# Kernel optimization log

Measured on AMD Instinct MI355X. Metric: run time of the kernel, lower is better.

## Reference

```python
import jax, jax.numpy as jnp
import numpy as np

N = 50000      # nodes
E = 800000     # edges (avg degree 16)
F_IN = 128
HID = 128
C = 40
EPS = 1e-5     # BatchNorm1d eps


def setup_inputs() -> dict:
    key = jax.random.key(0)
    ks = jax.random.split(key, 8)

    def glorot(k, shape):
        lim = np.sqrt(6.0 / (shape[0] + shape[1])).astype(np.float32)
        return jax.random.uniform(k, shape, jnp.float32, -lim, lim)

    inp = {
        "features": jax.random.normal(ks[0], (N, F_IN), jnp.float32),
        "edge_index": jax.random.randint(ks[1], (2, E), 0, N, jnp.int32),
        "W1": glorot(ks[2], (F_IN, HID)), "b1": jnp.zeros((HID,), jnp.float32),
        "gamma1": jnp.ones((HID,), jnp.float32), "beta1": jnp.zeros((HID,), jnp.float32),
        "W2": glorot(ks[3], (HID, HID)), "b2": jnp.zeros((HID,), jnp.float32),
        "gamma2": jnp.ones((HID,), jnp.float32), "beta2": jnp.zeros((HID,), jnp.float32),
        "W3": glorot(ks[4], (HID, C)), "b3": jnp.zeros((C,), jnp.float32),
    }
    return inp


def _gcn_norm(edge_index):
    # Add self-loops and compute symmetric normalization D^-1/2 (A+I) D^-1/2
    loops = jnp.arange(N, dtype=edge_index.dtype)
    src = jnp.concatenate([edge_index[0], loops])
    dst = jnp.concatenate([edge_index[1], loops])
    deg = jax.ops.segment_sum(jnp.ones((E + N,), jnp.float32), dst, num_segments=N)
    dinv = jax.lax.rsqrt(jnp.maximum(deg, 1.0))
    return src, dst, dinv[src] * dinv[dst]  # per-edge norm coefficient


def _gcn_conv(x, W, b, src, dst, norm):
    h = x @ W                                   # [N, out]
    msg = h[src] * norm[:, None]                # gather + scale, [E+N, out]
    return jax.ops.segment_sum(msg, dst, num_segments=N) + b


def _bn(x, gamma, beta):
    # training-mode BatchNorm1d over the node axis (biased variance)
    mu = jnp.mean(x, axis=0)
    var = jnp.mean(jnp.square(x - mu), axis=0)
    return (x - mu) * jax.lax.rsqrt(var + EPS) * gamma + beta


def reference(features, edge_index, W1, b1, gamma1, beta1, W2, b2, gamma2, beta2, W3, b3):
    src, dst, norm = _gcn_norm(edge_index)
    h = jax.nn.relu(_bn(_gcn_conv(features, W1, b1, src, dst, norm), gamma1, beta1))
    h = jax.nn.relu(_bn(_gcn_conv(h, W2, b2, src, dst, norm), gamma2, beta2))
    h = _gcn_conv(h, W3, b3, src, dst, norm)
    return jax.nn.log_softmax(h, axis=-1)
```

## Files before the change

kernel.cpp:

```cpp
#include <hip/hip_runtime.h>
#include <math.h>

#define FEAT 128
#define NCLS 40
#define BN_EPS 1e-5f
#define CAP 64

typedef unsigned short u16;
typedef unsigned int u32;
typedef __attribute__((ext_vector_type(8))) short bf16x8;
typedef __attribute__((ext_vector_type(4))) float f32x4;

__device__ inline u32 f2b2(float a, float b) {
    u32 ua = __float_as_uint(a), ub = __float_as_uint(b);
    ua = (ua + 0x7fffu + ((ua >> 16) & 1u)) >> 16;
    ub = (ub + 0x7fffu + ((ub >> 16) & 1u)) >> 16;
    return ua | (ub << 16);
}
__device__ inline u16 f2b1(float a) {
    u32 ua = __float_as_uint(a);
    return (u16)((ua + 0x7fffu + ((ua >> 16) & 1u)) >> 16);
}
__device__ inline float b2f(u16 u) { return __uint_as_float((u32)u << 16); }
__device__ inline float blo(u32 u) { return __uint_as_float(u << 16); }
__device__ inline float bhi(u32 u) { return __uint_as_float(u & 0xffff0000u); }

__device__ inline void b8acc(uint4 u, float w, float* a) {
    a[0] = fmaf(w, blo(u.x), a[0]); a[1] = fmaf(w, bhi(u.x), a[1]);
    a[2] = fmaf(w, blo(u.y), a[2]); a[3] = fmaf(w, bhi(u.y), a[3]);
    a[4] = fmaf(w, blo(u.z), a[4]); a[5] = fmaf(w, bhi(u.z), a[5]);
    a[6] = fmaf(w, blo(u.w), a[6]); a[7] = fmaf(w, bhi(u.w), a[7]);
}


__device__ inline void stage_wt(const float* __restrict__ W, u16* Wt) {
    const float4* W4 = (const float4*)W;
#pragma unroll
    for (int i = 0; i < 16; ++i) {
        int li = threadIdx.x + i * 256;
        int k = li >> 5;
        int n0 = (li & 31) * 4;
        int s = k >> 5, quad = (k >> 3) & 3, koff = k & 7;
        int nt = n0 >> 4, nl0 = n0 & 15;
        int base = ((s * 8 + nt) * 64 + quad * 16) * 8 + koff;
        float4 w = W4[li];
        Wt[base + (nl0 + 0) * 8] = f2b1(w.x);
        Wt[base + (nl0 + 1) * 8] = f2b1(w.y);
        Wt[base + (nl0 + 2) * 8] = f2b1(w.z);
        Wt[base + (nl0 + 3) * 8] = f2b1(w.w);
    }
}

__device__ inline void stage_wt40(const float* __restrict__ W, u16* Wt) {
    for (int e = threadIdx.x; e < 12 * 64 * 8; e += 256) {
        int j = e & 7;
        int lane = (e >> 3) & 63;
        int tile = e >> 9;
        int s = tile / 3, nt = tile % 3;
        int n = nt * 16 + (lane & 15);
        int k = s * 32 + (lane >> 4) * 8 + j;
        float v = (n < NCLS) ? W[k * NCLS + n] : 0.f;
        Wt[e] = f2b1(v);
    }
}

__global__ __launch_bounds__(256) void k_init(
    const float* __restrict__ W1, const float* __restrict__ W2,
    const float* __restrict__ W3, u16* __restrict__ Wg,
    uint4* __restrict__ zbase, int zcount)
{
    int b = blockIdx.x;
    if (b == 0) stage_wt(W1, Wg);
    else if (b == 1) stage_wt(W2, Wg + 128 * 128);
    else if (b == 2) stage_wt40(W3, Wg + 2 * 128 * 128);
    else {
        int idx = (b - 3) * 256 + threadIdx.x;
        if (idx < zcount) zbase[idx] = make_uint4(0, 0, 0, 0);
    }
}

__device__ inline void mfma_core(const uint4* __restrict__ wt4, const bf16x8* bfrag,
                                 u16* __restrict__ Y, int node, int M, int nl, int quad) {
    int lane = quad * 16 + nl;
    f32x4 acc[8];
#pragma unroll
    for (int nt = 0; nt < 8; ++nt) acc[nt] = (f32x4){0.f, 0.f, 0.f, 0.f};
#pragma unroll
    for (int s = 0; s < 4; ++s) {
#pragma unroll
        for (int nt = 0; nt < 8; ++nt) {
            uint4 aw = wt4[(s * 8 + nt) * 64 + lane];
            bf16x8 af = *(bf16x8*)&aw;
            acc[nt] = __builtin_amdgcn_mfma_f32_16x16x32_bf16(af, bfrag[s], acc[nt], 0, 0, 0);
        }
    }
    if (node < M) {
#pragma unroll
        for (int nt = 0; nt < 8; ++nt) {
            uint2 o;
            o.x = f2b2(acc[nt][0], acc[nt][1]);
            o.y = f2b2(acc[nt][2], acc[nt][3]);
            *(uint2*)&Y[(size_t)node * 128 + nt * 16 + quad * 4] = o;
        }
    }
}


__global__ __launch_bounds__(256, 8) void k_l1_fill(
    const float* __restrict__ X, const u16* __restrict__ Wg, u16* __restrict__ Y, int M,
    const int* __restrict__ src, const int* __restrict__ dst,
    int* __restrict__ cnt, u16* __restrict__ col, int E,
    int gemmBlocks, int nchunks)
{
    if ((int)blockIdx.x < gemmBlocks) {
        int wv = threadIdx.x >> 6;
        int lane = threadIdx.x & 63;
        int nl = lane & 15, quad = lane >> 4;
        int node = blockIdx.x * 64 + wv * 16 + nl;

        bf16x8 bfrag[4];
        if (node < M) {
            const float4* xr = (const float4*)(X + (size_t)node * 128);
#pragma unroll
            for (int s = 0; s < 4; ++s) {
                float4 xa = xr[s * 8 + quad * 2];
                float4 xb = xr[s * 8 + quad * 2 + 1];
                uint4 bu;
                bu.x = f2b2(xa.x, xa.y); bu.y = f2b2(xa.z, xa.w);
                bu.z = f2b2(xb.x, xb.y); bu.w = f2b2(xb.z, xb.w);
                bfrag[s] = *(bf16x8*)&bu;
            }
        } else {
            uint4 z = make_uint4(0, 0, 0, 0);
#pragma unroll
            for (int s = 0; s < 4; ++s) bfrag[s] = *(bf16x8*)&z;
        }
        mfma_core((const uint4*)Wg, bfrag, Y, node, M, nl, quad);
    } else {
        int fb = blockIdx.x - gemmBlocks;
        int part = fb & 7;
        int chunk = fb >> 3;
        int lo = (int)(((long long)M * part) >> 3);
        int hi = (int)(((long long)M * (part + 1)) >> 3);
        int per = ((E + nchunks - 1) / nchunks + 7) & ~7;
        int e0 = chunk * per;
        int e1 = e0 + per; if (e1 > E) e1 = E;

        for (int eb = e0 + (int)threadIdx.x * 8; eb < e1; eb += 2048) {
            if (eb + 8 <= e1) {
                int4 da = *(const int4*)(dst + eb);
                int4 db = *(const int4*)(dst + eb + 4);
                int4 sa = *(const int4*)(src + eb);
                int4 sb = *(const int4*)(src + eb + 4);
                int dd[8] = {da.x, da.y, da.z, da.w, db.x, db.y, db.z, db.w};
                int ss[8] = {sa.x, sa.y, sa.z, sa.w, sb.x, sb.y, sb.z, sb.w};
#pragma unroll
                for (int k = 0; k < 8; ++k) {
                    int d = dd[k];
                    if (d >= lo && d < hi) {
                        int c = atomicAdd(&cnt[d], 1);
                        if (c < CAP) col[(size_t)d * CAP + c] = (u16)ss[k];
                    }
                }
            } else {
                for (int e = eb; e < e1; ++e) {
                    int d = dst[e];
                    if (d >= lo && d < hi) {
                        int c = atomicAdd(&cnt[d], 1);
                        if (c < CAP) col[(size_t)d * CAP + c] = (u16)src[e];
                    }
                }
            }
        }
    }
}


__global__ __launch_bounds__(256) void k_mfma_l2(
    const u16* __restrict__ X, const u16* __restrict__ Wg,
    const float* __restrict__ sums, const float* __restrict__ gamma,
    const float* __restrict__ beta, u16* __restrict__ Y, int M)
{
    __shared__ __align__(16) u16 Wt[128 * 128];
    __shared__ __align__(16) float scs[128], shs[128];

    if (threadIdx.x < 128) {
        int f = threadIdx.x;
        float inv_n = 1.f / (float)M;
        float mu = sums[f] * inv_n;
        float var = sums[128 + f] * inv_n - mu * mu;
        float rs = rsqrtf(var + BN_EPS);
        float sc = gamma[f] * rs;
        scs[f] = sc;
        shs[f] = beta[f] - mu * sc;
    }
    {
        uint4* d4 = (uint4*)Wt;
        const uint4* s4 = (const uint4*)Wg;
#pragma unroll
        for (int i = 0; i < 8; ++i) d4[threadIdx.x + i * 256] = s4[threadIdx.x + i * 256];
    }
    __syncthreads();

    int wv = threadIdx.x >> 6;
    int lane = threadIdx.x & 63;
    int nl = lane & 15, quad = lane >> 4;
    int node = blockIdx.x * 64 + wv * 16 + nl;

    bf16x8 bfrag[4];
    if (node < M) {
        const uint4* xr = (const uint4*)(X + (size_t)node * 128);
#pragma unroll
        for (int s = 0; s < 4; ++s) {
            int k0 = s * 32 + quad * 8;
            uint4 xu = xr[s * 4 + quad];
            float4 sc0 = *(const float4*)&scs[k0];
            float4 sc1 = *(const float4*)&scs[k0 + 4];
            float4 sh0 = *(const float4*)&shs[k0];
            float4 sh1 = *(const float4*)&shs[k0 + 4];
            float v0 = fmaxf(fmaf(blo(xu.x), sc0.x, sh0.x), 0.f);
            float v1 = fmaxf(fmaf(bhi(xu.x), sc0.y, sh0.y), 0.f);
            float v2 = fmaxf(fmaf(blo(xu.y), sc0.z, sh0.z), 0.f);
            float v3 = fmaxf(fmaf(bhi(xu.y), sc0.w, sh0.w), 0.f);
            float v4 = fmaxf(fmaf(blo(xu.z), sc1.x, sh1.x), 0.f);
            float v5 = fmaxf(fmaf(bhi(xu.z), sc1.y, sh1.y), 0.f);
            float v6 = fmaxf(fmaf(blo(xu.w), sc1.z, sh1.z), 0.f);
            float v7 = fmaxf(fmaf(bhi(xu.w), sc1.w, sh1.w), 0.f);
            uint4 bu;
            bu.x = f2b2(v0, v1); bu.y = f2b2(v2, v3);
            bu.z = f2b2(v4, v5); bu.w = f2b2(v6, v7);
            bfrag[s] = *(bf16x8*)&bu;
        }
    } else {
        uint4 z = make_uint4(0, 0, 0, 0);
#pragma unroll
        for (int s = 0; s < 4; ++s) bfrag[s] = *(bf16x8*)&z;
    }
    mfma_core((const uint4*)Wt, bfrag, Y, node, M, nl, quad);
}


__global__ __launch_bounds__(256) void k_mfma_l3(
    const u16* __restrict__ X, const u16* __restrict__ Wg,
    const float* __restrict__ sums, const float* __restrict__ gamma,
    const float* __restrict__ beta, u16* __restrict__ Y, int M)
{
    __shared__ __align__(16) u16 Wt[12 * 64 * 8];
    __shared__ __align__(16) float scs[128], shs[128];

    if (threadIdx.x < 128) {
        int f = threadIdx.x;
        float inv_n = 1.f / (float)M;
        float mu = sums[f] * inv_n;
        float var = sums[128 + f] * inv_n - mu * mu;
        float rs = rsqrtf(var + BN_EPS);
        float sc = gamma[f] * rs;
        scs[f] = sc;
        shs[f] = beta[f] - mu * sc;
    }
    {
        uint4* d4 = (uint4*)Wt;
        const uint4* s4 = (const uint4*)Wg;
#pragma unroll
        for (int i = 0; i < 3; ++i) d4[threadIdx.x + i * 256] = s4[threadIdx.x + i * 256];
    }
    __syncthreads();

    int wv = threadIdx.x >> 6;
    int lane = threadIdx.x & 63;
    int nl = lane & 15, quad = lane >> 4;
    int node = blockIdx.x * 64 + wv * 16 + nl;

    bf16x8 bfrag[4];
    if (node < M) {
        const uint4* xr = (const uint4*)(X + (size_t)node * 128);
#pragma unroll
        for (int s = 0; s < 4; ++s) {
            int k0 = s * 32 + quad * 8;
            uint4 xu = xr[s * 4 + quad];
            float4 sc0 = *(const float4*)&scs[k0];
            float4 sc1 = *(const float4*)&scs[k0 + 4];
            float4 sh0 = *(const float4*)&shs[k0];
            float4 sh1 = *(const float4*)&shs[k0 + 4];
            float v0 = fmaxf(fmaf(blo(xu.x), sc0.x, sh0.x), 0.f);
            float v1 = fmaxf(fmaf(bhi(xu.x), sc0.y, sh0.y), 0.f);
            float v2 = fmaxf(fmaf(blo(xu.y), sc0.z, sh0.z), 0.f);
            float v3 = fmaxf(fmaf(bhi(xu.y), sc0.w, sh0.w), 0.f);
            float v4 = fmaxf(fmaf(blo(xu.z), sc1.x, sh1.x), 0.f);
            float v5 = fmaxf(fmaf(bhi(xu.z), sc1.y, sh1.y), 0.f);
            float v6 = fmaxf(fmaf(blo(xu.w), sc1.z, sh1.z), 0.f);
            float v7 = fmaxf(fmaf(bhi(xu.w), sc1.w, sh1.w), 0.f);
            uint4 bu;
            bu.x = f2b2(v0, v1); bu.y = f2b2(v2, v3);
            bu.z = f2b2(v4, v5); bu.w = f2b2(v6, v7);
            bfrag[s] = *(bf16x8*)&bu;
        }
    } else {
        uint4 z = make_uint4(0, 0, 0, 0);
#pragma unroll
        for (int s = 0; s < 4; ++s) bfrag[s] = *(bf16x8*)&z;
    }

    const uint4* wt4 = (const uint4*)Wt;
    f32x4 acc[3];
#pragma unroll
    for (int nt = 0; nt < 3; ++nt) acc[nt] = (f32x4){0.f, 0.f, 0.f, 0.f};
#pragma unroll
    for (int s = 0; s < 4; ++s) {
#pragma unroll
        for (int nt = 0; nt < 3; ++nt) {
            uint4 aw = wt4[(s * 3 + nt) * 64 + lane];
            bf16x8 af = *(bf16x8*)&aw;
            acc[nt] = __builtin_amdgcn_mfma_f32_16x16x32_bf16(af, bfrag[s], acc[nt], 0, 0, 0);
        }
    }
    if (node < M) {
#pragma unroll
        for (int nt = 0; nt < 3; ++nt) {
            int c0 = nt * 16 + quad * 4;
            if (c0 < NCLS) {
                uint2 o;
                o.x = f2b2(acc[nt][0], acc[nt][1]);
                o.y = f2b2(acc[nt][2], acc[nt][3]);
                *(uint2*)&Y[(size_t)node * NCLS + c0] = o;
            }
        }
    }
}


__global__ __launch_bounds__(256) void k_agg128_bn(
    const u16* __restrict__ t, const int* __restrict__ cnt,
    const u16* __restrict__ col, const float* __restrict__ bias,
    u16* __restrict__ out, float* __restrict__ sums, int n)
{
    int wid = threadIdx.x >> 4;
    int lane = threadIdx.x & 15;
    float4 bA = ((const float4*)bias)[lane * 2];
    float4 bB = ((const float4*)bias)[lane * 2 + 1];

    float bs[8], bq[8];
#pragma unroll
    for (int k = 0; k < 8; ++k) { bs[k] = 0.f; bq[k] = 0.f; }

    for (int i0 = blockIdx.x * 16; i0 < n; i0 += gridDim.x * 16) {
        int i = i0 + wid;
        if (i < n) {
            int c = cnt[i];
            int deg = c < CAP ? c : CAP;
            int beg = i * CAP, end = beg + deg;
            float di = rsqrtf((float)(c + 1));

            float a[8];
            {
                uint4 su = ((const uint4*)(t + (size_t)i * 128))[lane];
                a[0] = di * blo(su.x); a[1] = di * bhi(su.x);
                a[2] = di * blo(su.y); a[3] = di * bhi(su.y);
                a[4] = di * blo(su.z); a[5] = di * bhi(su.z);
                a[6] = di * blo(su.w); a[7] = di * bhi(su.w);
            }

            int j = beg;
            for (; j + 7 < end; j += 8) {
                int s[8]; int sc[8]; uint4 v[8];
#pragma unroll
                for (int k = 0; k < 8; ++k) s[k] = (int)col[j + k];
#pragma unroll
                for (int k = 0; k < 8; ++k) {
                    sc[k] = cnt[s[k]];
                    v[k] = ((const uint4*)(t + (size_t)s[k] * 128))[lane];
                }
#pragma unroll
                for (int k = 0; k < 8; ++k) b8acc(v[k], rsqrtf((float)(sc[k] + 1)), a);
            }
            for (; j < end; ++j) {
                int s0 = (int)col[j];
                float w0 = rsqrtf((float)(cnt[s0] + 1));
                uint4 v = ((const uint4*)(t + (size_t)s0 * 128))[lane];
                b8acc(v, w0, a);
            }

            float vv[8];
            vv[0] = fmaf(di, a[0], bA.x); vv[1] = fmaf(di, a[1], bA.y);
            vv[2] = fmaf(di, a[2], bA.z); vv[3] = fmaf(di, a[3], bA.w);
            vv[4] = fmaf(di, a[4], bB.x); vv[5] = fmaf(di, a[5], bB.y);
            vv[6] = fmaf(di, a[6], bB.z); vv[7] = fmaf(di, a[7], bB.w);
            uint4 o;
            o.x = f2b2(vv[0], vv[1]); o.y = f2b2(vv[2], vv[3]);
            o.z = f2b2(vv[4], vv[5]); o.w = f2b2(vv[6], vv[7]);
            ((uint4*)(out + (size_t)i * 128))[lane] = o;
#pragma unroll
            for (int k = 0; k < 8; ++k) {
                bs[k] += vv[k];
                bq[k] = fmaf(vv[k], vv[k], bq[k]);
            }
        }
    }

    __shared__ float red[16][128];
#pragma unroll
    for (int k = 0; k < 8; ++k) red[wid][lane * 8 + k] = bs[k];
    __syncthreads();
    if (threadIdx.x < 128) {
        float v = 0.f;
#pragma unroll
        for (int w = 0; w < 16; ++w) v += red[w][threadIdx.x];
        atomicAdd(&sums[threadIdx.x], v);
    }
    __syncthreads();
#pragma unroll
    for (int k = 0; k < 8; ++k) red[wid][lane * 8 + k] = bq[k];
    __syncthreads();
    if (threadIdx.x < 128) {
        float v = 0.f;
#pragma unroll
        for (int w = 0; w < 16; ++w) v += red[w][threadIdx.x];
        atomicAdd(&sums[128 + threadIdx.x], v);
    }
}


__global__ __launch_bounds__(256) void k_agg40(
    const u16* __restrict__ t, const int* __restrict__ cnt,
    const u16* __restrict__ col, const float* __restrict__ bias,
    float* __restrict__ out, int n)
{
    int i = blockIdx.x * 32 + (threadIdx.x >> 3);
    if (i >= n) return;
    int l = threadIdx.x & 7;
    bool act = l < 5;
    int c = cnt[i];
    int deg = c < CAP ? c : CAP;
    int beg = i * CAP, end = beg + deg;
    float di = rsqrtf((float)(c + 1));

    float a[8] = {0.f, 0.f, 0.f, 0.f, 0.f, 0.f, 0.f, 0.f};
    if (act) {
        uint4 su = ((const uint4*)(t + (size_t)i * NCLS))[l];
        a[0] = di * blo(su.x); a[1] = di * bhi(su.x);
        a[2] = di * blo(su.y); a[3] = di * bhi(su.y);
        a[4] = di * blo(su.z); a[5] = di * bhi(su.z);
        a[6] = di * blo(su.w); a[7] = di * bhi(su.w);
    }
    int j = beg;
    for (; j + 7 < end; j += 8) {
        int s[8]; int sc[8]; uint4 v[8];
#pragma unroll
        for (int k = 0; k < 8; ++k) s[k] = (int)col[j + k];
#pragma unroll
        for (int k = 0; k < 8; ++k) {
            sc[k] = cnt[s[k]];
            v[k] = act ? ((const uint4*)(t + (size_t)s[k] * NCLS))[l]
                       : make_uint4(0, 0, 0, 0);
        }
#pragma unroll
        for (int k = 0; k < 8; ++k) b8acc(v[k], rsqrtf((float)(sc[k] + 1)), a);
    }
    for (; j < end; ++j) {
        int s0 = (int)col[j];
        float w0 = rsqrtf((float)(cnt[s0] + 1));
        uint4 v = act ? ((const uint4*)(t + (size_t)s0 * NCLS))[l]
                      : make_uint4(0, 0, 0, 0);
        b8acc(v, w0, a);
    }

    float v[8];
    float m = -INFINITY;
    if (act) {
        float4 b0 = *(const float4*)(bias + l * 8);
        float4 b1 = *(const float4*)(bias + l * 8 + 4);
        v[0] = fmaf(di, a[0], b0.x); v[1] = fmaf(di, a[1], b0.y);
        v[2] = fmaf(di, a[2], b0.z); v[3] = fmaf(di, a[3], b0.w);
        v[4] = fmaf(di, a[4], b1.x); v[5] = fmaf(di, a[5], b1.y);
        v[6] = fmaf(di, a[6], b1.z); v[7] = fmaf(di, a[7], b1.w);
#pragma unroll
        for (int k = 0; k < 8; ++k) m = fmaxf(m, v[k]);
    }
#pragma unroll
    for (int d = 1; d < 8; d <<= 1) m = fmaxf(m, __shfl_xor(m, d, 8));
    float es = 0.f;
    if (act) {
#pragma unroll
        for (int k = 0; k < 8; ++k) es += expf(v[k] - m);
    }
#pragma unroll
    for (int d = 1; d < 8; d <<= 1) es += __shfl_xor(es, d, 8);
    float ls = logf(es);
    if (act) {
        float4 o0, o1;
        o0.x = v[0] - m - ls; o0.y = v[1] - m - ls;
        o0.z = v[2] - m - ls; o0.w = v[3] - m - ls;
        o1.x = v[4] - m - ls; o1.y = v[5] - m - ls;
        o1.z = v[6] - m - ls; o1.w = v[7] - m - ls;
        *(float4*)(out + (size_t)i * NCLS + l * 8) = o0;
        *(float4*)(out + (size_t)i * NCLS + l * 8 + 4) = o1;
    }
}


extern "C" void kernel_launch(void* const* d_in, const int* in_sizes, int n_in,
                              void* d_out, int out_size, void* d_ws, size_t ws_size,
                              hipStream_t stream) {
    const float* features = (const float*)d_in[0];
    const int* edge_index = (const int*)d_in[1];
    const float* W1 = (const float*)d_in[2];
    const float* b1 = (const float*)d_in[3];
    const float* gamma1 = (const float*)d_in[4];
    const float* beta1 = (const float*)d_in[5];
    const float* W2 = (const float*)d_in[6];
    const float* b2 = (const float*)d_in[7];
    const float* gamma2 = (const float*)d_in[8];
    const float* beta2 = (const float*)d_in[9];
    const float* W3 = (const float*)d_in[10];
    const float* b3 = (const float*)d_in[11];
    float* out = (float*)d_out;

    int n = in_sizes[0] / FEAT;
    int E = in_sizes[1] / 2;

    char* p = (char*)d_ws;
    auto alloc = [&](size_t bytes) -> void* {
        void* r = (void*)p;
        p += (bytes + 255) & ~(size_t)255;
        return r;
    };
    int* cnt     = (int*)alloc((size_t)n * 4);
    float* sums  = (float*)alloc(512 * 4);
    size_t zspan = (size_t)((char*)(sums + 512) - (char*)cnt);
    u16* colb    = (u16*)alloc((size_t)n * CAP * 2);
    u16* hb      = (u16*)alloc((size_t)n * 128 * 2);
    u16* ab      = (u16*)alloc((size_t)n * 128 * 2);
    u16* wgb     = (u16*)alloc((size_t)(2 * 128 * 128 + 12 * 64 * 8) * 2);

    float* sums1 = sums;
    float* sums2 = sums + 256;
    u16* Wg1 = wgb;
    u16* Wg2 = wgb + 128 * 128;
    u16* Wg3 = wgb + 2 * 128 * 128;

    const int* e_src = edge_index;
    const int* e_dst = edge_index + E;

    int gb64 = (n + 63) / 64;
    int gb16 = (n + 15) / 16;
    int gb32 = (n + 31) / 32;
    int aggGrid = gb16 < 1024 ? gb16 : 1024;

    int zcount = (int)(zspan / 16);
    int zblocks = (zcount + 255) / 256;
    k_init<<<3 + zblocks, 256, 0, stream>>>(W1, W2, W3, wgb, (uint4*)cnt, zcount);

    int nchunks = 160;
    k_l1_fill<<<gb64 + nchunks * 8, 256, 0, stream>>>(features, Wg1, hb, n,
                                                      e_src, e_dst, cnt, colb, E,
                                                      gb64, nchunks);

    k_agg128_bn<<<aggGrid, 256, 0, stream>>>(hb, cnt, colb, b1, ab, sums1, n);

    k_mfma_l2<<<gb64, 256, 0, stream>>>(ab, Wg2, sums1, gamma1, beta1, hb, n);
    k_agg128_bn<<<aggGrid, 256, 0, stream>>>(hb, cnt, colb, b2, ab, sums2, n);

    k_mfma_l3<<<gb64, 256, 0, stream>>>(ab, Wg3, sums2, gamma2, beta2, hb, n);
    k_agg40<<<gb32, 256, 0, stream>>>(hb, cnt, colb, b3, out, n);
}
```

Before: 299.7 us.

## Compress edge indices to u16, double node tile in L2 GEMM, resize agg grid

Edge src/dst arrays are packed to 16-bit indices once in the init kernel, so the CSR fill pass reads half the bytes, using nontemporal loads. The layer-2 MFMA kernel now processes 128 nodes per block, reusing each shared-memory weight fragment for two node tiles, with the BN-prep code factored into a helper. The aggregation grid is no longer capped at 1024 blocks. The packing adds an extra pass over the edge array and relies on node ids fitting in 16 bits, which holds for N=50000. The larger GEMM tile raises register pressure.

```diff
diff --git a/kernel.cpp b/kernel.cpp
--- a/kernel.cpp
+++ b/kernel.cpp
@@ -10,6 +10,7 @@
 typedef unsigned int u32;
 typedef __attribute__((ext_vector_type(8))) short bf16x8;
 typedef __attribute__((ext_vector_type(4))) float f32x4;
+typedef __attribute__((ext_vector_type(4))) u32 u32x4;
 
 __device__ inline u32 f2b2(float a, float b) {
     u32 ua = __float_as_uint(a), ub = __float_as_uint(b);
@@ -67,15 +68,30 @@
 __global__ __launch_bounds__(256) void k_init(
     const float* __restrict__ W1, const float* __restrict__ W2,
     const float* __restrict__ W3, u16* __restrict__ Wg,
-    uint4* __restrict__ zbase, int zcount)
+    uint4* __restrict__ zbase, int zcount, int zblocks,
+    const int* __restrict__ edges, u16* __restrict__ ew, int twoE)
 {
     int b = blockIdx.x;
     if (b == 0) stage_wt(W1, Wg);
     else if (b == 1) stage_wt(W2, Wg + 128 * 128);
     else if (b == 2) stage_wt40(W3, Wg + 2 * 128 * 128);
-    else {
+    else if (b < 3 + zblocks) {
         int idx = (b - 3) * 256 + threadIdx.x;
         if (idx < zcount) zbase[idx] = make_uint4(0, 0, 0, 0);
+    } else {
+        int idx = ((b - 3 - zblocks) * 256 + threadIdx.x) * 8;
+        if (idx + 8 <= twoE) {
+            int4 a = *(const int4*)(edges + idx);
+            int4 c = *(const int4*)(edges + idx + 4);
+            uint4 o;
+            o.x = (u32)(a.x & 0xffff) | ((u32)a.y << 16);
+            o.y = (u32)(a.z & 0xffff) | ((u32)a.w << 16);
+            o.z = (u32)(c.x & 0xffff) | ((u32)c.y << 16);
+            o.w = (u32)(c.z & 0xffff) | ((u32)c.w << 16);
+            *(uint4*)(ew + idx) = o;
+        } else {
+            for (int e = idx; e < twoE; ++e) ew[e] = (u16)edges[e];
+        }
     }
 }
 
@@ -108,7 +124,7 @@
 
 __global__ __launch_bounds__(256, 8) void k_l1_fill(
     const float* __restrict__ X, const u16* __restrict__ Wg, u16* __restrict__ Y, int M,
-    const int* __restrict__ src, const int* __restrict__ dst,
+    const u16* __restrict__ srcw, const u16* __restrict__ dstw,
     int* __restrict__ cnt, u16* __restrict__ col, int E,
     int gemmBlocks, int nchunks)
 {
@@ -148,26 +164,30 @@
 
         for (int eb = e0 + (int)threadIdx.x * 8; eb < e1; eb += 2048) {
             if (eb + 8 <= e1) {
-                int4 da = *(const int4*)(dst + eb);
-                int4 db = *(const int4*)(dst + eb + 4);
-                int4 sa = *(const int4*)(src + eb);
-                int4 sb = *(const int4*)(src + eb + 4);
-                int dd[8] = {da.x, da.y, da.z, da.w, db.x, db.y, db.z, db.w};
-                int ss[8] = {sa.x, sa.y, sa.z, sa.w, sb.x, sb.y, sb.z, sb.w};
+                u32x4 du = __builtin_nontemporal_load((const u32x4*)(dstw + eb));
+                u32x4 su = __builtin_nontemporal_load((const u32x4*)(srcw + eb));
+                int dd[8] = {(int)(du.x & 0xffffu), (int)(du.x >> 16),
+                             (int)(du.y & 0xffffu), (int)(du.y >> 16),
+                             (int)(du.z & 0xffffu), (int)(du.z >> 16),
+                             (int)(du.w & 0xffffu), (int)(du.w >> 16)};
+                u16 ss[8] = {(u16)(su.x & 0xffffu), (u16)(su.x >> 16),
+                             (u16)(su.y & 0xffffu), (u16)(su.y >> 16),
+                             (u16)(su.z & 0xffffu), (u16)(su.z >> 16),
+                             (u16)(su.w & 0xffffu), (u16)(su.w >> 16)};
 #pragma unroll
                 for (int k = 0; k < 8; ++k) {
                     int d = dd[k];
                     if (d >= lo && d < hi) {
                         int c = atomicAdd(&cnt[d], 1);
-                        if (c < CAP) col[(size_t)d * CAP + c] = (u16)ss[k];
+                        if (c < CAP) col[(size_t)d * CAP + c] = ss[k];
                     }
                 }
             } else {
                 for (int e = eb; e < e1; ++e) {
-                    int d = dst[e];
+                    int d = (int)dstw[e];
                     if (d >= lo && d < hi) {
                         int c = atomicAdd(&cnt[d], 1);
-                        if (c < CAP) col[(size_t)d * CAP + c] = (u16)src[e];
+                        if (c < CAP) col[(size_t)d * CAP + c] = srcw[e];
                     }
                 }
             }
@@ -176,38 +196,9 @@
 }
 
 
-__global__ __launch_bounds__(256) void k_mfma_l2(
-    const u16* __restrict__ X, const u16* __restrict__ Wg,
-    const float* __restrict__ sums, const float* __restrict__ gamma,
-    const float* __restrict__ beta, u16* __restrict__ Y, int M)
-{
-    __shared__ __align__(16) u16 Wt[128 * 128];
-    __shared__ __align__(16) float scs[128], shs[128];
-
-    if (threadIdx.x < 128) {
-        int f = threadIdx.x;
-        float inv_n = 1.f / (float)M;
-        float mu = sums[f] * inv_n;
-        float var = sums[128 + f] * inv_n - mu * mu;
-        float rs = rsqrtf(var + BN_EPS);
-        float sc = gamma[f] * rs;
-        scs[f] = sc;
-        shs[f] = beta[f] - mu * sc;
-    }
-    {
-        uint4* d4 = (uint4*)Wt;
-        const uint4* s4 = (const uint4*)Wg;
-#pragma unroll
-        for (int i = 0; i < 8; ++i) d4[threadIdx.x + i * 256] = s4[threadIdx.x + i * 256];
-    }
-    __syncthreads();
-
-    int wv = threadIdx.x >> 6;
-    int lane = threadIdx.x & 63;
-    int nl = lane & 15, quad = lane >> 4;
-    int node = blockIdx.x * 64 + wv * 16 + nl;
-
-    bf16x8 bfrag[4];
+__device__ inline void build_bfrag_bn(const u16* __restrict__ X, int node, int M,
+                                      int quad, const float* scs, const float* shs,
+                                      bf16x8* bfrag) {
     if (node < M) {
         const uint4* xr = (const uint4*)(X + (size_t)node * 128);
 #pragma unroll
@@ -236,16 +227,14 @@
 #pragma unroll
         for (int s = 0; s < 4; ++s) bfrag[s] = *(bf16x8*)&z;
     }
-    mfma_core((const uint4*)Wt, bfrag, Y, node, M, nl, quad);
-}
-
-
-__global__ __launch_bounds__(256) void k_mfma_l3(
+}
+
+__global__ __launch_bounds__(256, 2) void k_mfma_l2(
     const u16* __restrict__ X, const u16* __restrict__ Wg,
     const float* __restrict__ sums, const float* __restrict__ gamma,
     const float* __restrict__ beta, u16* __restrict__ Y, int M)
 {
-    __shared__ __align__(16) u16 Wt[12 * 64 * 8];
+    __shared__ __align__(16) u16 Wt[128 * 128];
     __shared__ __align__(16) float scs[128], shs[128];
 
     if (threadIdx.x < 128) {
@@ -262,6 +251,80 @@
         uint4* d4 = (uint4*)Wt;
         const uint4* s4 = (const uint4*)Wg;
 #pragma unroll
+        for (int i = 0; i < 8; ++i) d4[threadIdx.x + i * 256] = s4[threadIdx.x + i * 256];
+    }
+    __syncthreads();
+
+    int wv = threadIdx.x >> 6;
+    int lane = threadIdx.x & 63;
+    int nl = lane & 15, quad = lane >> 4;
+    int nodeA = blockIdx.x * 128 + wv * 16 + nl;
+    int nodeB = nodeA + 64;
+
+    bf16x8 bfragA[4], bfragB[4];
+    build_bfrag_bn(X, nodeA, M, quad, scs, shs, bfragA);
+    build_bfrag_bn(X, nodeB, M, quad, scs, shs, bfragB);
+
+    const uint4* wt4 = (const uint4*)Wt;
+    f32x4 accA[8], accB[8];
+#pragma unroll
+    for (int nt = 0; nt < 8; ++nt) {
+        accA[nt] = (f32x4){0.f, 0.f, 0.f, 0.f};
+        accB[nt] = (f32x4){0.f, 0.f, 0.f, 0.f};
+    }
+#pragma unroll
+    for (int s = 0; s < 4; ++s) {
+#pragma unroll
+        for (int nt = 0; nt < 8; ++nt) {
+            uint4 aw = wt4[(s * 8 + nt) * 64 + lane];
+            bf16x8 af = *(bf16x8*)&aw;
+            accA[nt] = __builtin_amdgcn_mfma_f32_16x16x32_bf16(af, bfragA[s], accA[nt], 0, 0, 0);
+            accB[nt] = __builtin_amdgcn_mfma_f32_16x16x32_bf16(af, bfragB[s], accB[nt], 0, 0, 0);
+        }
+    }
+    if (nodeA < M) {
+#pragma unroll
+        for (int nt = 0; nt < 8; ++nt) {
+            uint2 o;
+            o.x = f2b2(accA[nt][0], accA[nt][1]);
+            o.y = f2b2(accA[nt][2], accA[nt][3]);
+            *(uint2*)&Y[(size_t)nodeA * 128 + nt * 16 + quad * 4] = o;
+        }
+    }
+    if (nodeB < M) {
+#pragma unroll
+        for (int nt = 0; nt < 8; ++nt) {
+            uint2 o;
+            o.x = f2b2(accB[nt][0], accB[nt][1]);
+            o.y = f2b2(accB[nt][2], accB[nt][3]);
+            *(uint2*)&Y[(size_t)nodeB * 128 + nt * 16 + quad * 4] = o;
+        }
+    }
+}
+
+
+__global__ __launch_bounds__(256) void k_mfma_l3(
+    const u16* __restrict__ X, const u16* __restrict__ Wg,
+    const float* __restrict__ sums, const float* __restrict__ gamma,
+    const float* __restrict__ beta, u16* __restrict__ Y, int M)
+{
+    __shared__ __align__(16) u16 Wt[12 * 64 * 8];
+    __shared__ __align__(16) float scs[128], shs[128];
+
+    if (threadIdx.x < 128) {
+        int f = threadIdx.x;
+        float inv_n = 1.f / (float)M;
+        float mu = sums[f] * inv_n;
+        float var = sums[128 + f] * inv_n - mu * mu;
+        float rs = rsqrtf(var + BN_EPS);
+        float sc = gamma[f] * rs;
+        scs[f] = sc;
+        shs[f] = beta[f] - mu * sc;
+    }
+    {
+        uint4* d4 = (uint4*)Wt;
+        const uint4* s4 = (const uint4*)Wg;
+#pragma unroll
         for (int i = 0; i < 3; ++i) d4[threadIdx.x + i * 256] = s4[threadIdx.x + i * 256];
     }
     __syncthreads();
@@ -272,34 +335,7 @@
     int node = blockIdx.x * 64 + wv * 16 + nl;
 
     bf16x8 bfrag[4];
-    if (node < M) {
-        const uint4* xr = (const uint4*)(X + (size_t)node * 128);
-#pragma unroll
-        for (int s = 0; s < 4; ++s) {
-            int k0 = s * 32 + quad * 8;
-            uint4 xu = xr[s * 4 + quad];
-            float4 sc0 = *(const float4*)&scs[k0];
-            float4 sc1 = *(const float4*)&scs[k0 + 4];
-            float4 sh0 = *(const float4*)&shs[k0];
-            float4 sh1 = *(const float4*)&shs[k0 + 4];
-            float v0 = fmaxf(fmaf(blo(xu.x), sc0.x, sh0.x), 0.f);
-            float v1 = fmaxf(fmaf(bhi(xu.x), sc0.y, sh0.y), 0.f);
-            float v2 = fmaxf(fmaf(blo(xu.y), sc0.z, sh0.z), 0.f);
-            float v3 = fmaxf(fmaf(bhi(xu.y), sc0.w, sh0.w), 0.f);
-            float v4 = fmaxf(fmaf(blo(xu.z), sc1.x, sh1.x), 0.f);
-            float v5 = fmaxf(fmaf(bhi(xu.z), sc1.y, sh1.y), 0.f);
-            float v6 = fmaxf(fmaf(blo(xu.w), sc1.z, sh1.z), 0.f);
-            float v7 = fmaxf(fmaf(bhi(xu.w), sc1.w, sh1.w), 0.f);
-            uint4 bu;
-            bu.x = f2b2(v0, v1); bu.y = f2b2(v2, v3);
-            bu.z = f2b2(v4, v5); bu.w = f2b2(v6, v7);
-            bfrag[s] = *(bf16x8*)&bu;
-        }
-    } else {
-        uint4 z = make_uint4(0, 0, 0, 0);
-#pragma unroll
-        for (int s = 0; s < 4; ++s) bfrag[s] = *(bf16x8*)&z;
-    }
+    build_bfrag_bn(X, node, M, quad, scs, shs, bfrag);
 
     const uint4* wt4 = (const uint4*)Wt;
     f32x4 acc[3];
@@ -531,34 +567,38 @@
     u16* hb      = (u16*)alloc((size_t)n * 128 * 2);
     u16* ab      = (u16*)alloc((size_t)n * 128 * 2);
     u16* wgb     = (u16*)alloc((size_t)(2 * 128 * 128 + 12 * 64 * 8) * 2);
+    u16* ew      = (u16*)alloc((size_t)2 * E * 2);
 
     float* sums1 = sums;
     float* sums2 = sums + 256;
     u16* Wg1 = wgb;
     u16* Wg2 = wgb + 128 * 128;
     u16* Wg3 = wgb + 2 * 128 * 128;
-
-    const int* e_src = edge_index;
-    const int* e_dst = edge_index + E;
+    u16* srcw = ew;
+    u16* dstw = ew + E;
 
     int gb64 = (n + 63) / 64;
+    int gb128 = (n + 127) / 128;
     int gb16 = (n + 15) / 16;
     int gb32 = (n + 31) / 32;
-    int aggGrid = gb16 < 1024 ? gb16 : 1024;
 
     int zcount = (int)(zspan / 16);
     int zblocks = (zcount + 255) / 256;
-    k_init<<<3 + zblocks, 256, 0, stream>>>(W1, W2, W3, wgb, (uint4*)cnt, zcount);
+    int twoE = 2 * E;
+    int cblocks = (twoE / 8 + 255) / 256;
+    k_init<<<3 + zblocks + cblocks, 256, 0, stream>>>(W1, W2, W3, wgb,
+                                                      (uint4*)cnt, zcount, zblocks,
+                                                      edge_index, ew, twoE);
 
     int nchunks = 160;
     k_l1_fill<<<gb64 + nchunks * 8, 256, 0, stream>>>(features, Wg1, hb, n,
-                                                      e_src, e_dst, cnt, colb, E,
+                                                      srcw, dstw, cnt, colb, E,
                                                       gb64, nchunks);
 
-    k_agg128_bn<<<aggGrid, 256, 0, stream>>>(hb, cnt, colb, b1, ab, sums1, n);
-
-    k_mfma_l2<<<gb64, 256, 0, stream>>>(ab, Wg2, sums1, gamma1, beta1, hb, n);
-    k_agg128_bn<<<aggGrid, 256, 0, stream>>>(hb, cnt, colb, b2, ab, sums2, n);
+    k_agg128_bn<<<gb16, 256, 0, stream>>>(hb, cnt, colb, b1, ab, sums1, n);
+
+    k_mfma_l2<<<gb128, 256, 0, stream>>>(ab, Wg2, sums1, gamma1, beta1, hb, n);
+    k_agg128_bn<<<gb16, 256, 0, stream>>>(hb, cnt, colb, b2, ab, sums2, n);
 
     k_mfma_l3<<<gb64, 256, 0, stream>>>(ab, Wg3, sums2, gamma2, beta2, hb, n);
     k_agg40<<<gb32, 256, 0, stream>>>(hb, cnt, colb, b3, out, n);
```

Result: slower. 376.7 us (+25.7%).
